# Kernel optimization log

Measured on AMD Instinct MI355X. Metric: run time of the kernel, lower is better.

## Reference

```python
import jax, jax.numpy as jnp
import numpy as np

B, CIN, L = 4, 128, 2048
D_MODEL, D_STATE, EXPAND, HEADDIM, NGROUPS = 256, 16, 3, 3, 1
D_INNER = EXPAND * D_MODEL            # 768
NHEADS = D_INNER // HEADDIM           # 256
CONV_DIM = D_INNER + 2 * NGROUPS * D_STATE   # 800
D_IN_PROJ = 2 * D_INNER + 2 * NGROUPS * D_STATE + NHEADS  # 1824
K_PROJ, D_CONV = 4, 4
EPS = 1e-5


def setup_inputs() -> dict:
    key = jax.random.key(0)
    ks = jax.random.split(key, 9)
    x = jax.random.normal(ks[0], (B, CIN, L), jnp.float32)
    proj_w = jax.random.normal(ks[1], (D_MODEL, CIN, K_PROJ), jnp.float32) / np.float32(np.sqrt(CIN * K_PROJ))
    in_proj_w = jax.random.normal(ks[2], (D_IN_PROJ, D_MODEL), jnp.float32) / np.float32(np.sqrt(D_MODEL))
    conv_w = jax.random.normal(ks[3], (CONV_DIM, 1, D_CONV), jnp.float32) / np.float32(np.sqrt(D_CONV))
    conv_b = jax.random.normal(ks[4], (CONV_DIM,), jnp.float32) * 0.01
    # dt_bias = inverse-softplus of dt ~ LogUniform[1e-3, 1e-1] (mamba2 init)
    u = jax.random.uniform(ks[5], (NHEADS,), jnp.float32)
    dt = jnp.exp(u * np.float32(np.log(0.1) - np.log(1e-3)) + np.float32(np.log(1e-3)))
    dt_bias = dt + jnp.log(-jnp.expm1(-dt))
    A_log = jnp.log(1.0 + 15.0 * jax.random.uniform(ks[6], (NHEADS,), jnp.float32))  # A in [-16,-1]
    D_skip = jnp.ones((NHEADS,), jnp.float32)
    norm_w = jnp.ones((D_INNER,), jnp.float32)
    out_proj_w = jax.random.normal(ks[7], (D_MODEL, D_INNER), jnp.float32) / np.float32(np.sqrt(D_INNER))
    return {"x": x, "proj_w": proj_w, "in_proj_w": in_proj_w, "conv_w": conv_w,
            "conv_b": conv_b, "dt_bias": dt_bias, "A_log": A_log, "D_skip": D_skip,
            "norm_w": norm_w, "out_proj_w": out_proj_w}


def _forward(x, proj_w, in_proj_w, conv_w, conv_b, dt_bias, A_log, D_skip, norm_w, out_proj_w):
    # outer Conv1d, padding='same' (k=4 -> left 1, right 2), no bias: (B,CIN,L)->(B,D_MODEL,L)
    h = jax.lax.conv_general_dilated(x, proj_w, (1,), [(1, 2)],
                                     dimension_numbers=("NCH", "OIH", "NCH"))
    u = h.transpose(0, 2, 1)                          # (B, L, d_model)
    zxbcdt = jnp.einsum("bld,ed->ble", u, in_proj_w)  # (B, L, 1824)
    z = zxbcdt[..., :D_INNER]                                     # (B,L,768)
    xBC = zxbcdt[..., D_INNER:D_INNER + CONV_DIM]                 # (B,L,800)
    dt = zxbcdt[..., D_INNER + CONV_DIM:]                         # (B,L,256)
    dt = jax.nn.softplus(dt + dt_bias)
    # depthwise causal conv (pad d_conv-1 on left) + SiLU
    xBC_c = jax.lax.conv_general_dilated(xBC.transpose(0, 2, 1), conv_w, (1,), [(D_CONV - 1, 0)],
                                         feature_group_count=CONV_DIM,
                                         dimension_numbers=("NCH", "OIH", "NCH"))
    xBC = jax.nn.silu(xBC_c + conv_b[None, :, None]).transpose(0, 2, 1)  # (B,L,800)
    xs = xBC[..., :D_INNER].reshape(B, L, NHEADS, HEADDIM)        # (B,L,H,P)
    Bm = xBC[..., D_INNER:D_INNER + D_STATE]                      # (B,L,N) (ngroups=1)
    Cm = xBC[..., D_INNER + D_STATE:]                             # (B,L,N)
    A = -jnp.exp(A_log)                                           # (H,)

    def step(hst, inp):
        dt_t, x_t, B_t, C_t = inp                 # (B,H),(B,H,P),(B,N),(B,N)
        dA = jnp.exp(dt_t * A)[:, :, None, None]  # (B,H,1,1)
        hst = dA * hst + jnp.einsum("bh,bhp,bn->bhpn", dt_t, x_t, B_t)
        y_t = jnp.einsum("bhpn,bn->bhp", hst, C_t)
        return hst, y_t

    h0 = jnp.zeros((B, NHEADS, HEADDIM, D_STATE), x.dtype)
    _, ys = jax.lax.scan(step, h0, (dt.transpose(1, 0, 2), xs.transpose(1, 0, 2, 3),
                                    Bm.transpose(1, 0, 2), Cm.transpose(1, 0, 2)))
    y = ys.transpose(1, 0, 2, 3) + D_skip[None, None, :, None] * xs   # (B,L,H,P)
    y = y.reshape(B, L, D_INNER)
    # gated RMSNorm: gate first, then normalize (norm_before_gate=False)
    y = y * jax.nn.silu(z)
    y = y * jax.lax.rsqrt(jnp.mean(y * y, axis=-1, keepdims=True) + EPS) * norm_w
    out = jnp.einsum("ble,de->bld", y, out_proj_w)   # (B,L,d_model)
    return out.transpose(0, 2, 1)                    # (B,d_model,L)


def reference(x, proj_w, in_proj_w, conv_w, conv_b, dt_bias, A_log, D_skip, norm_w, out_proj_w):
    return _forward(x, proj_w, in_proj_w, conv_w, conv_b, dt_bias, A_log, D_skip, norm_w, out_proj_w)
```

## Files before the change

kernel.cpp:

```cpp
#include <hip/hip_runtime.h>
#include <hip/hip_fp16.h>
#include <math.h>

#define B_     4
#define CIN    128
#define LEN    2048
#define DMODEL 256
#define DSTATE 16
#define NHEADS 256
#define DINNER 768
#define CONVDIM 800
#define DINPROJ 1824
#define EPS_   1e-5f
#define CHUNK  64
#define NCHUNK 32

typedef _Float16 f16x8 __attribute__((ext_vector_type(8)));
typedef float    f32x4 __attribute__((ext_vector_type(4)));

__device__ __forceinline__ float silu_(float x){ return x / (1.0f + __expf(-x)); }
__device__ __forceinline__ float softplus_(float x){
    return x > 0.f ? x + log1pf(__expf(-x)) : log1pf(__expf(x));
}

__device__ __forceinline__ void gl2lds16(const _Float16* g, _Float16* l){
    __builtin_amdgcn_global_load_lds(
        (const __attribute__((address_space(1))) void*)g,
        (__attribute__((address_space(3))) void*)l, 16, 0, 0);
}

__global__ __launch_bounds__(256) void k_f2h(const float* __restrict__ a,
                                             _Float16* __restrict__ o, int n){
    for (int i = blockIdx.x * 256 + threadIdx.x; i < n; i += gridDim.x * 256)
        o[i] = (_Float16)a[i];
}

__global__ __launch_bounds__(256) void k_im2col(const float* __restrict__ x,
                                                _Float16* __restrict__ xcol){
    __shared__ float xs[CIN][68];
    int blk = blockIdx.x;
    int b  = blk >> 5;
    int l0 = (blk & 31) << 6;
    const float* xb = x + (size_t)b * CIN * LEN;
    for (int idx = threadIdx.x; idx < CIN * 67; idx += 256){
        int ci = idx / 67, j = idx % 67;
        int gl = l0 - 1 + j;
        xs[ci][j] = (gl >= 0 && gl < LEN) ? xb[ci * LEN + gl] : 0.f;
    }
    __syncthreads();
    #pragma unroll
    for (int v = 0; v < 16; v++){
        int id = v * 256 + threadIdx.x;
        int rl = id >> 6, c = id & 63;
        f16x8 pk;
        #pragma unroll
        for (int e = 0; e < 8; e++){
            int ci = c * 2 + (e >> 2), k = e & 3;
            pk[e] = (_Float16)xs[ci][rl + k];
        }
        *(f16x8*)&xcol[((size_t)(b * LEN + l0 + rl)) * 512 + c * 8] = pk;
    }
}

template<int K, int EPI>
__global__ __launch_bounds__(256) void k_gemm(const _Float16* __restrict__ A,
                                              const _Float16* __restrict__ Bw,
                                              const float* __restrict__ dt_bias,
                                              _Float16* __restrict__ o_u,
                                              _Float16* __restrict__ o_z,
                                              _Float16* __restrict__ o_xbc,
                                              _Float16* __restrict__ o_dt,
                                              float* __restrict__ o_f){
    __shared__ __align__(16) _Float16 As[128 * 32];
    __shared__ __align__(16) _Float16 Bs[128 * 32];
    int tid  = threadIdx.x;
    int wv   = tid >> 6;
    int lane = tid & 63;
    int quad = lane >> 4;
    int l16  = lane & 15;
    int m0 = blockIdx.x * 128;
    int n0 = blockIdx.y * 128;
    int wm = (wv >> 1) * 64;
    int wn = (wv & 1) * 64;
    int srow = lane >> 2;
    int scol = (lane & 3) * 8;

    f32x4 acc[4][4];
    #pragma unroll
    for (int i = 0; i < 4; i++)
        #pragma unroll
        for (int j = 0; j < 4; j++)
            acc[i][j] = (f32x4){0.f, 0.f, 0.f, 0.f};

    for (int k0 = 0; k0 < K; k0 += 32){
        #pragma unroll
        for (int j = 0; j < 2; j++){
            int ar = m0 + wv * 32 + j * 16 + srow;
            gl2lds16(A + (size_t)ar * K + k0 + scol,
                     &As[(wv * 32 + j * 16) * 32]);
            int nr = n0 + wv * 32 + j * 16 + srow;
            if (EPI == 1) nr = nr > (DINPROJ - 1) ? (DINPROJ - 1) : nr;
            gl2lds16(Bw + (size_t)nr * K + k0 + scol,
                     &Bs[(wv * 32 + j * 16) * 32]);
        }
        __syncthreads();
        f16x8 af[4], bf[4];
        #pragma unroll
        for (int i = 0; i < 4; i++)
            af[i] = *(const f16x8*)&As[(wm + i * 16 + l16) * 32 + quad * 8];
        #pragma unroll
        for (int j = 0; j < 4; j++)
            bf[j] = *(const f16x8*)&Bs[(wn + j * 16 + l16) * 32 + quad * 8];
        #pragma unroll
        for (int i = 0; i < 4; i++)
            #pragma unroll
            for (int j = 0; j < 4; j++)
                acc[i][j] = __builtin_amdgcn_mfma_f32_16x16x32_f16(
                                af[i], bf[j], acc[i][j], 0, 0, 0);
        __syncthreads();
    }

    if (EPI == 0){
        #pragma unroll
        for (int j = 0; j < 4; j++){
            int col = n0 + wn + j * 16 + l16;
            #pragma unroll
            for (int i = 0; i < 4; i++){
                int row = m0 + wm + i * 16 + quad * 4;
                #pragma unroll
                for (int r = 0; r < 4; r++)
                    o_u[(size_t)(row + r) * DMODEL + col] = (_Float16)acc[i][j][r];
            }
        }
    } else if (EPI == 1){
        #pragma unroll
        for (int j = 0; j < 4; j++){
            int col = n0 + wn + j * 16 + l16;
            if (col < DINNER){
                #pragma unroll
                for (int i = 0; i < 4; i++){
                    int row = m0 + wm + i * 16 + quad * 4;
                    #pragma unroll
                    for (int r = 0; r < 4; r++)
                        o_z[(size_t)(row + r) * DINNER + col] = (_Float16)acc[i][j][r];
                }
            } else if (col < DINNER + CONVDIM){
                int cc = col - DINNER;
                #pragma unroll
                for (int i = 0; i < 4; i++){
                    int row = m0 + wm + i * 16 + quad * 4;
                    #pragma unroll
                    for (int r = 0; r < 4; r++)
                        o_xbc[(size_t)(row + r) * CONVDIM + cc] = (_Float16)acc[i][j][r];
                }
            } else if (col < DINPROJ){
                int hh = col - (DINNER + CONVDIM);
                float bias = dt_bias[hh];
                #pragma unroll
                for (int i = 0; i < 4; i++){
                    int row = m0 + wm + i * 16 + quad * 4;
                    #pragma unroll
                    for (int r = 0; r < 4; r++)
                        o_dt[(size_t)(row + r) * NHEADS + hh] =
                            (_Float16)softplus_(acc[i][j][r] + bias);
                }
            }
        }
    } else {
        #pragma unroll
        for (int i = 0; i < 4; i++){
            int row = m0 + wm + i * 16 + quad * 4;
            int b = row >> 11, l = row & (LEN - 1);
            #pragma unroll
            for (int j = 0; j < 4; j++){
                int d = n0 + wn + j * 16 + l16;
                *(f32x4*)&o_f[(((size_t)(b * DMODEL + d)) << 11) + l] = acc[i][j];
            }
        }
    }
}

__global__ __launch_bounds__(256) void k_dwconv(const __half* __restrict__ xbc,
                                                const float* __restrict__ cw,
                                                const float* __restrict__ cb,
                                                __half* __restrict__ xcc){
    int idx = blockIdx.x * 256 + threadIdx.x;
    int c = idx % CONVDIM;
    int r = idx / CONVDIM;
    int l = r & (LEN - 1);
    float4 wv = *(const float4*)(cw + c * 4);
    float acc = cb[c];
    if (l >= 3){
        const __half* base = xbc + (size_t)(r - 3) * CONVDIM + c;
        acc += __half2float(base[0]) * wv.x + __half2float(base[CONVDIM]) * wv.y +
               __half2float(base[2 * CONVDIM]) * wv.z + __half2float(base[3 * CONVDIM]) * wv.w;
    } else {
        const float wk[4] = {wv.x, wv.y, wv.z, wv.w};
        for (int k = 0; k < 4; k++){
            int t = l - 3 + k;
            if (t >= 0) acc += __half2float(xbc[(size_t)(r + k - 3) * CONVDIM + c]) * wk[k];
        }
    }
    xcc[idx] = __float2half(silu_(acc));
}

__global__ __launch_bounds__(64) void k_scanA(const __half* __restrict__ dtb,
                                              const __half* __restrict__ xcc,
                                              const float* __restrict__ A_log,
                                              __half* __restrict__ cstate,
                                              float* __restrict__ dsum){
    int blk = blockIdx.x;
    int c  = blk & (NCHUNK - 1);
    int hg = (blk >> 5) & 63;
    int b  = blk >> 11;
    int lane = threadIdx.x;
    int hl = lane >> 4;
    int n  = lane & 15;
    int h  = hg * 4 + hl;
    int c0 = h * 3;
    float A = -__expf(A_log[h]);
    int t0 = c * CHUNK;
    const __half* xr  = xcc + ((size_t)b * LEN + t0) * CONVDIM;
    const __half* dtp = dtb + ((size_t)b * LEN + t0) * NHEADS + h;
    float h0 = 0.f, h1 = 0.f, h2 = 0.f, sdt = 0.f;
    for (int t = 0; t < CHUNK; t++){
        float vx0 = __half2float(xr[c0]);
        float vx1 = __half2float(xr[c0 + 1]);
        float vx2 = __half2float(xr[c0 + 2]);
        float vB  = __half2float(xr[DINNER + n]);
        float cdt = __half2float(dtp[(size_t)t * NHEADS]);
        float dA  = __expf(cdt * A);
        float dtB = cdt * vB;
        h0 = fmaf(h0, dA, vx0 * dtB);
        h1 = fmaf(h1, dA, vx1 * dtB);
        h2 = fmaf(h2, dA, vx2 * dtB);
        sdt += cdt;
        xr += CONVDIM;
    }
    size_t sbase = (((size_t)(b * NHEADS + h)) * NCHUNK + c) * 48;
    cstate[sbase + n]      = __float2half(h0);
    cstate[sbase + 16 + n] = __float2half(h1);
    cstate[sbase + 32 + n] = __float2half(h2);
    if (n == 0) dsum[(size_t)(b * NHEADS + h) * NCHUNK + c] = __expf(A * sdt);
}

__global__ __launch_bounds__(64) void k_scanB(__half* __restrict__ cstate,
                                              const float* __restrict__ dsum){
    int bh = blockIdx.x;
    int lane = threadIdx.x;
    if (lane >= 48) return;
    __half* st = cstate + (size_t)bh * NCHUNK * 48 + lane;
    const float* dd = dsum + (size_t)bh * NCHUNK;
    float H = 0.f;
    for (int c = 0; c < NCHUNK; c++){
        float d = dd[c];
        float s = __half2float(st[(size_t)c * 48]);
        st[(size_t)c * 48] = __float2half(H);
        H = fmaf(H, d, s);
    }
}

__global__ __launch_bounds__(64) void k_scanC(const __half* __restrict__ dtb,
                                              const __half* __restrict__ xcc,
                                              const float* __restrict__ A_log,
                                              const float* __restrict__ D_skip,
                                              const __half* __restrict__ cstate,
                                              __half* __restrict__ y){
    int blk = blockIdx.x;
    int c  = blk & (NCHUNK - 1);
    int hg = (blk >> 5) & 63;
    int b  = blk >> 11;
    int lane = threadIdx.x;
    int hl = lane >> 4;
    int n  = lane & 15;
    int h  = hg * 4 + hl;
    int c0 = h * 3;
    float A   = -__expf(A_log[h]);
    float Dsk = D_skip[h];
    int t0 = c * CHUNK;
    const __half* xr  = xcc + ((size_t)b * LEN + t0) * CONVDIM;
    const __half* dtp = dtb + ((size_t)b * LEN + t0) * NHEADS + h;
    size_t sbase = (((size_t)(b * NHEADS + h)) * NCHUNK + c) * 48;
    float h0 = __half2float(cstate[sbase + n]);
    float h1 = __half2float(cstate[sbase + 16 + n]);
    float h2 = __half2float(cstate[sbase + 32 + n]);
    __half* yp = y + ((size_t)b * LEN + t0) * DINNER + c0;
    for (int t = 0; t < CHUNK; t++){
        float vx0 = __half2float(xr[c0]);
        float vx1 = __half2float(xr[c0 + 1]);
        float vx2 = __half2float(xr[c0 + 2]);
        float vB  = __half2float(xr[DINNER + n]);
        float vC  = __half2float(xr[DINNER + DSTATE + n]);
        float cdt = __half2float(dtp[(size_t)t * NHEADS]);
        float dA  = __expf(cdt * A);
        float dtB = cdt * vB;
        h0 = fmaf(h0, dA, vx0 * dtB);
        h1 = fmaf(h1, dA, vx1 * dtB);
        h2 = fmaf(h2, dA, vx2 * dtB);
        float p0 = h0 * vC, p1 = h1 * vC, p2 = h2 * vC;
        #pragma unroll
        for (int m = 1; m < 16; m <<= 1){
            p0 += __shfl_xor(p0, m, 64);
            p1 += __shfl_xor(p1, m, 64);
            p2 += __shfl_xor(p2, m, 64);
        }
        if (n < 3){
            float pv = (n == 0) ? p0 : ((n == 1) ? p1 : p2);
            float xv = (n == 0) ? vx0 : ((n == 1) ? vx1 : vx2);
            yp[n] = __float2half(fmaf(Dsk, xv, pv));
        }
        xr += CONVDIM;
        yp += DINNER;
    }
}

__global__ __launch_bounds__(256) void k_norm(__half* __restrict__ y,
                                              const __half* __restrict__ z,
                                              const float* __restrict__ nw){
    __shared__ float wsum[4];
    size_t r = blockIdx.x;
    int tid = threadIdx.x;
    const __half* zr = z + r * DINNER;
    __half* yr = y + r * DINNER;
    int e0 = tid, e1 = tid + 256, e2 = tid + 512;
    float t0 = __half2float(yr[e0]) * silu_(__half2float(zr[e0]));
    float t1 = __half2float(yr[e1]) * silu_(__half2float(zr[e1]));
    float t2 = __half2float(yr[e2]) * silu_(__half2float(zr[e2]));
    float ss = t0 * t0 + t1 * t1 + t2 * t2;
    #pragma unroll
    for (int m = 1; m < 64; m <<= 1) ss += __shfl_xor(ss, m, 64);
    if ((tid & 63) == 0) wsum[tid >> 6] = ss;
    __syncthreads();
    float tot = wsum[0] + wsum[1] + wsum[2] + wsum[3];
    float sc = rsqrtf(tot / (float)DINNER + EPS_);
    yr[e0] = __float2half(t0 * sc * nw[e0]);
    yr[e1] = __float2half(t1 * sc * nw[e1]);
    yr[e2] = __float2half(t2 * sc * nw[e2]);
}

extern "C" void kernel_launch(void* const* d_in, const int* in_sizes, int n_in,
                              void* d_out, int out_size, void* d_ws, size_t ws_size,
                              hipStream_t stream) {
    const float* x          = (const float*)d_in[0];
    const float* proj_w     = (const float*)d_in[1];
    const float* in_proj_w  = (const float*)d_in[2];
    const float* conv_w     = (const float*)d_in[3];
    const float* conv_b     = (const float*)d_in[4];
    const float* dt_bias    = (const float*)d_in[5];
    const float* A_log      = (const float*)d_in[6];
    const float* D_skip     = (const float*)d_in[7];
    const float* norm_w     = (const float*)d_in[8];
    const float* out_proj_w = (const float*)d_in[9];
    float* out = (float*)d_out;

    char* ob = (char*)d_out;
    _Float16* pw_h  = (_Float16*)ob;
    _Float16* ipw_h = (_Float16*)(ob + 262144);

    char* wsb = (char*)d_ws;
    _Float16* xcol  = (_Float16*)(wsb);
    _Float16* u_h   = (_Float16*)(wsb + 8388608);
    __half*   xcc_h = (__half*)(wsb);
    __half*   z_h   = (__half*)(wsb + 13107200);
    __half*   xbc_h = (__half*)(wsb + 25690112);
    __half*   y_h   = xbc_h;
    __half*   dt_h  = (__half*)(wsb + 38797312);
    __half*   cstate= (__half*)(wsb + 42991616);
    float*    dsum  = (float*)(wsb + 46137344);
    _Float16* opw_h = (_Float16*)(wsb + 46268416);

    k_f2h   <<<64, 256, 0, stream>>>(proj_w,     pw_h,  DMODEL * CIN * 4);
    k_f2h   <<<64, 256, 0, stream>>>(in_proj_w,  ipw_h, DINPROJ * DMODEL);
    k_f2h   <<<64, 256, 0, stream>>>(out_proj_w, opw_h, DMODEL * DINNER);
    k_im2col<<<128, 256, 0, stream>>>(x, xcol);
    k_gemm<512, 0><<<dim3(64, 2), 256, 0, stream>>>(xcol, pw_h, nullptr,
        u_h, nullptr, nullptr, nullptr, nullptr);
    k_gemm<256, 1><<<dim3(64, 15), 256, 0, stream>>>(u_h, ipw_h, dt_bias,
        nullptr, (_Float16*)z_h, (_Float16*)xbc_h, (_Float16*)dt_h, nullptr);
    k_dwconv<<<25600, 256, 0, stream>>>(xbc_h, conv_w, conv_b, xcc_h);
    k_scanA <<<8192, 64, 0, stream>>>(dt_h, xcc_h, A_log, cstate, dsum);
    k_scanB <<<1024, 64, 0, stream>>>(cstate, dsum);
    k_scanC <<<8192, 64, 0, stream>>>(dt_h, xcc_h, A_log, D_skip, cstate, y_h);
    k_norm  <<<8192, 256, 0, stream>>>(y_h, z_h, norm_w);
    k_gemm<768, 2><<<dim3(64, 2), 256, 0, stream>>>((const _Float16*)y_h, opw_h,
        nullptr, nullptr, nullptr, nullptr, nullptr, out);
}
```

Before: 318.4 us.

## Fuse intra-chunk output into chunk-state scan and add parallel inter-chunk correction

The first scan pass now also produces the intra-chunk output y (from a zero initial state), staging B/C, x and dt for the chunk in shared memory rather than doing strided global loads every step. The second sequential scan pass over all chunks is replaced by a parallel correction kernel: one thread per timestep takes a prefix sum of dt, computes the decay from the chunk's carried-in state, and adds C·H·decay to y. This removes one full sequential recurrence pass, at the cost of an extra read-modify-write of y in fp16 and a shuffle reduction added to the first pass.

```diff
diff --git a/kernel.cpp b/kernel.cpp
--- a/kernel.cpp
+++ b/kernel.cpp
@@ -204,11 +204,16 @@
     xcc[idx] = __float2half(silu_(acc));
 }
 
-__global__ __launch_bounds__(64) void k_scanA(const __half* __restrict__ dtb,
-                                              const __half* __restrict__ xcc,
-                                              const float* __restrict__ A_log,
-                                              __half* __restrict__ cstate,
-                                              float* __restrict__ dsum){
+__global__ __launch_bounds__(64) void k_scanAY(const __half* __restrict__ dtb,
+                                               const __half* __restrict__ xcc,
+                                               const float* __restrict__ A_log,
+                                               const float* __restrict__ D_skip,
+                                               __half* __restrict__ y,
+                                               __half* __restrict__ cstate,
+                                               float* __restrict__ dsum){
+    __shared__ __align__(16) __half sBC[CHUNK * 32];
+    __shared__ __align__(8)  __half sx[CHUNK * 12];
+    __shared__ __align__(8)  __half sdt4[CHUNK * 4];
     int blk = blockIdx.x;
     int c  = blk & (NCHUNK - 1);
     int hg = (blk >> 5) & 63;
@@ -217,25 +222,60 @@
     int hl = lane >> 4;
     int n  = lane & 15;
     int h  = hg * 4 + hl;
-    int c0 = h * 3;
-    float A = -__expf(A_log[h]);
     int t0 = c * CHUNK;
-    const __half* xr  = xcc + ((size_t)b * LEN + t0) * CONVDIM;
-    const __half* dtp = dtb + ((size_t)b * LEN + t0) * NHEADS + h;
+    size_t row0 = (size_t)(b * LEN + t0);
+
+    {
+        const char* g = (const char*)xcc + (row0 * CONVDIM + DINNER) * 2;
+        int tt = lane >> 2, q = lane & 3;
+        #pragma unroll
+        for (int i = 0; i < 4; i++)
+            gl2lds16((const _Float16*)(g + (size_t)(i * 16 + tt) * (CONVDIM * 2) + q * 16),
+                     (_Float16*)&sBC[i * 512]);
+    }
+    {
+        const char* gx = (const char*)xcc + (row0 + lane) * (CONVDIM * 2) + hg * 24;
+        uint2 a0 = *(const uint2*)(gx);
+        uint2 a1 = *(const uint2*)(gx + 8);
+        uint2 a2 = *(const uint2*)(gx + 16);
+        *(uint2*)&sx[lane * 12]     = a0;
+        *(uint2*)&sx[lane * 12 + 4] = a1;
+        *(uint2*)&sx[lane * 12 + 8] = a2;
+        const char* gd = (const char*)dtb + (row0 + lane) * (NHEADS * 2) + hg * 8;
+        *(uint2*)&sdt4[lane * 4] = *(const uint2*)gd;
+    }
+    __syncthreads();
+
+    float A   = -__expf(A_log[h]);
+    float Dsk = D_skip[h];
     float h0 = 0.f, h1 = 0.f, h2 = 0.f, sdt = 0.f;
+    __half* yp = y + row0 * DINNER + hg * 12 + hl * 3;
+    #pragma unroll 4
     for (int t = 0; t < CHUNK; t++){
-        float vx0 = __half2float(xr[c0]);
-        float vx1 = __half2float(xr[c0 + 1]);
-        float vx2 = __half2float(xr[c0 + 2]);
-        float vB  = __half2float(xr[DINNER + n]);
-        float cdt = __half2float(dtp[(size_t)t * NHEADS]);
+        float vx0 = __half2float(sx[t * 12 + hl * 3]);
+        float vx1 = __half2float(sx[t * 12 + hl * 3 + 1]);
+        float vx2 = __half2float(sx[t * 12 + hl * 3 + 2]);
+        float vB  = __half2float(sBC[t * 32 + n]);
+        float vC  = __half2float(sBC[t * 32 + 16 + n]);
+        float cdt = __half2float(sdt4[t * 4 + hl]);
         float dA  = __expf(cdt * A);
         float dtB = cdt * vB;
         h0 = fmaf(h0, dA, vx0 * dtB);
         h1 = fmaf(h1, dA, vx1 * dtB);
         h2 = fmaf(h2, dA, vx2 * dtB);
         sdt += cdt;
-        xr += CONVDIM;
+        float p0 = h0 * vC, p1 = h1 * vC, p2 = h2 * vC;
+        p0 += __shfl_xor(p0, 1, 64); p1 += __shfl_xor(p1, 1, 64); p2 += __shfl_xor(p2, 1, 64);
+        p0 += __shfl_xor(p0, 2, 64); p1 += __shfl_xor(p1, 2, 64); p2 += __shfl_xor(p2, 2, 64);
+        int g = n & 3;
+        float q = (g == 1) ? p1 : ((g == 2) ? p2 : p0);
+        q += __shfl_xor(q, 4, 64);
+        q += __shfl_xor(q, 8, 64);
+        if (n < 3){
+            float xv = (n == 0) ? vx0 : ((n == 1) ? vx1 : vx2);
+            yp[n] = __float2half(fmaf(Dsk, xv, q));
+        }
+        yp += DINNER;
     }
     size_t sbase = (((size_t)(b * NHEADS + h)) * NCHUNK + c) * 48;
     cstate[sbase + n]      = __float2half(h0);
@@ -260,58 +300,43 @@
     }
 }
 
-__global__ __launch_bounds__(64) void k_scanC(const __half* __restrict__ dtb,
-                                              const __half* __restrict__ xcc,
-                                              const float* __restrict__ A_log,
-                                              const float* __restrict__ D_skip,
-                                              const __half* __restrict__ cstate,
-                                              __half* __restrict__ y){
-    int blk = blockIdx.x;
-    int c  = blk & (NCHUNK - 1);
-    int hg = (blk >> 5) & 63;
-    int b  = blk >> 11;
+__global__ __launch_bounds__(64) void k_corr(const __half* __restrict__ dtb,
+                                             const __half* __restrict__ xcc,
+                                             const float* __restrict__ A_log,
+                                             const __half* __restrict__ cstate,
+                                             __half* __restrict__ y){
+    __shared__ float sH[48];
+    int c = 1 + blockIdx.x;
+    int h = blockIdx.y;
+    int b = blockIdx.z;
     int lane = threadIdx.x;
-    int hl = lane >> 4;
-    int n  = lane & 15;
-    int h  = hg * 4 + hl;
-    int c0 = h * 3;
-    float A   = -__expf(A_log[h]);
-    float Dsk = D_skip[h];
+    size_t sbase = (((size_t)(b * NHEADS + h)) * NCHUNK + c) * 48;
+    if (lane < 48) sH[lane] = __half2float(cstate[sbase + lane]);
+    float A = -__expf(A_log[h]);
     int t0 = c * CHUNK;
-    const __half* xr  = xcc + ((size_t)b * LEN + t0) * CONVDIM;
-    const __half* dtp = dtb + ((size_t)b * LEN + t0) * NHEADS + h;
-    size_t sbase = (((size_t)(b * NHEADS + h)) * NCHUNK + c) * 48;
-    float h0 = __half2float(cstate[sbase + n]);
-    float h1 = __half2float(cstate[sbase + 16 + n]);
-    float h2 = __half2float(cstate[sbase + 32 + n]);
-    __half* yp = y + ((size_t)b * LEN + t0) * DINNER + c0;
-    for (int t = 0; t < CHUNK; t++){
-        float vx0 = __half2float(xr[c0]);
-        float vx1 = __half2float(xr[c0 + 1]);
-        float vx2 = __half2float(xr[c0 + 2]);
-        float vB  = __half2float(xr[DINNER + n]);
-        float vC  = __half2float(xr[DINNER + DSTATE + n]);
-        float cdt = __half2float(dtp[(size_t)t * NHEADS]);
-        float dA  = __expf(cdt * A);
-        float dtB = cdt * vB;
-        h0 = fmaf(h0, dA, vx0 * dtB);
-        h1 = fmaf(h1, dA, vx1 * dtB);
-        h2 = fmaf(h2, dA, vx2 * dtB);
-        float p0 = h0 * vC, p1 = h1 * vC, p2 = h2 * vC;
-        #pragma unroll
-        for (int m = 1; m < 16; m <<= 1){
-            p0 += __shfl_xor(p0, m, 64);
-            p1 += __shfl_xor(p1, m, 64);
-            p2 += __shfl_xor(p2, m, 64);
-        }
-        if (n < 3){
-            float pv = (n == 0) ? p0 : ((n == 1) ? p1 : p2);
-            float xv = (n == 0) ? vx0 : ((n == 1) ? vx1 : vx2);
-            yp[n] = __float2half(fmaf(Dsk, xv, pv));
-        }
-        xr += CONVDIM;
-        yp += DINNER;
-    }
+    size_t row = (size_t)(b * LEN + t0 + lane);
+    float cdt = __half2float(dtb[row * NHEADS + h]);
+    float cum = cdt;
+    #pragma unroll
+    for (int m = 1; m < 64; m <<= 1){
+        float v = __shfl_up(cum, m, 64);
+        if (lane >= m) cum += v;
+    }
+    float decay = __expf(A * cum);
+    __syncthreads();
+    const __half* Cp = xcc + row * CONVDIM + DINNER + DSTATE;
+    float c0 = 0.f, c1 = 0.f, c2 = 0.f;
+    #pragma unroll
+    for (int nn = 0; nn < 16; nn++){
+        float cv = __half2float(Cp[nn]);
+        c0 = fmaf(cv, sH[nn],      c0);
+        c1 = fmaf(cv, sH[16 + nn], c1);
+        c2 = fmaf(cv, sH[32 + nn], c2);
+    }
+    __half* yy = y + row * DINNER + h * 3;
+    yy[0] = __float2half(fmaf(decay, c0, __half2float(yy[0])));
+    yy[1] = __float2half(fmaf(decay, c1, __half2float(yy[1])));
+    yy[2] = __float2half(fmaf(decay, c2, __half2float(yy[2])));
 }
 
 __global__ __launch_bounds__(256) void k_norm(__half* __restrict__ y,
@@ -378,9 +403,9 @@
     k_gemm<256, 1><<<dim3(64, 15), 256, 0, stream>>>(u_h, ipw_h, dt_bias,
         nullptr, (_Float16*)z_h, (_Float16*)xbc_h, (_Float16*)dt_h, nullptr);
     k_dwconv<<<25600, 256, 0, stream>>>(xbc_h, conv_w, conv_b, xcc_h);
-    k_scanA <<<8192, 64, 0, stream>>>(dt_h, xcc_h, A_log, cstate, dsum);
+    k_scanAY<<<8192, 64, 0, stream>>>(dt_h, xcc_h, A_log, D_skip, y_h, cstate, dsum);
     k_scanB <<<1024, 64, 0, stream>>>(cstate, dsum);
-    k_scanC <<<8192, 64, 0, stream>>>(dt_h, xcc_h, A_log, D_skip, cstate, y_h);
+    k_corr  <<<dim3(NCHUNK - 1, NHEADS, B_), 64, 0, stream>>>(dt_h, xcc_h, A_log, cstate, y_h);
     k_norm  <<<8192, 256, 0, stream>>>(y_h, z_h, norm_w);
     k_gemm<768, 2><<<dim3(64, 2), 256, 0, stream>>>((const _Float16*)y_h, opw_h,
         nullptr, nullptr, nullptr, nullptr, nullptr, out);
```

After: 408.0 us. 1.28x slower.

## Replace sequential chunk scan with SSD-style intra-band quadratic form and correction pass

Applied to the files above, without the earlier changes.

Replaces the per-timestep sequential scan kernels with a chunked SSD formulation. Each block loads a 64-row band and 64 heads into LDS. It computes cumulative decay, C·B dot products, and the intra-band output with 16-step sub-segments plus sub-segment state carries. It also writes band end states and per-row decay factors (E0, stored in the output buffer as scratch) so a separate correction kernel can add the inter-band contribution. The D-skip term moves into the norm kernel. This trades the latency-bound serial recurrence over tiny 64-thread blocks for parallel, arithmetic-heavy work, at the cost of more exp evaluations, high register pressure, and extra E0 traffic.

```diff
diff --git a/kernel.cpp b/kernel.cpp
--- a/kernel.cpp
+++ b/kernel.cpp
@@ -12,10 +12,12 @@
 #define CONVDIM 800
 #define DINPROJ 1824
 #define EPS_   1e-5f
-#define CHUNK  64
-#define NCHUNK 32
+#define BAND   64
+#define NBAND  32
+#define SEG    16
 
 typedef _Float16 f16x8 __attribute__((ext_vector_type(8)));
+typedef _Float16 f16x4 __attribute__((ext_vector_type(4)));
 typedef float    f32x4 __attribute__((ext_vector_type(4)));
 
 __device__ __forceinline__ float silu_(float x){ return x / (1.0f + __expf(-x)); }
@@ -204,44 +206,236 @@
     xcc[idx] = __float2half(silu_(acc));
 }
 
-__global__ __launch_bounds__(64) void k_scanA(const __half* __restrict__ dtb,
-                                              const __half* __restrict__ xcc,
-                                              const float* __restrict__ A_log,
-                                              __half* __restrict__ cstate,
-                                              float* __restrict__ dsum){
-    int blk = blockIdx.x;
-    int c  = blk & (NCHUNK - 1);
-    int hg = (blk >> 5) & 63;
-    int b  = blk >> 11;
-    int lane = threadIdx.x;
-    int hl = lane >> 4;
-    int n  = lane & 15;
-    int h  = hg * 4 + hl;
-    int c0 = h * 3;
-    float A = -__expf(A_log[h]);
-    int t0 = c * CHUNK;
-    const __half* xr  = xcc + ((size_t)b * LEN + t0) * CONVDIM;
-    const __half* dtp = dtb + ((size_t)b * LEN + t0) * NHEADS + h;
-    float h0 = 0.f, h1 = 0.f, h2 = 0.f, sdt = 0.f;
-    for (int t = 0; t < CHUNK; t++){
-        float vx0 = __half2float(xr[c0]);
-        float vx1 = __half2float(xr[c0 + 1]);
-        float vx2 = __half2float(xr[c0 + 2]);
-        float vB  = __half2float(xr[DINNER + n]);
-        float cdt = __half2float(dtp[(size_t)t * NHEADS]);
-        float dA  = __expf(cdt * A);
-        float dtB = cdt * vB;
-        h0 = fmaf(h0, dA, vx0 * dtB);
-        h1 = fmaf(h1, dA, vx1 * dtB);
-        h2 = fmaf(h2, dA, vx2 * dtB);
-        sdt += cdt;
-        xr += CONVDIM;
-    }
-    size_t sbase = (((size_t)(b * NHEADS + h)) * NCHUNK + c) * 48;
-    cstate[sbase + n]      = __float2half(h0);
-    cstate[sbase + 16 + n] = __float2half(h1);
-    cstate[sbase + 32 + n] = __float2half(h2);
-    if (n == 0) dsum[(size_t)(b * NHEADS + h) * NCHUNK + c] = __expf(A * sdt);
+__global__ __launch_bounds__(256) void k_y(const __half* __restrict__ dtb,
+                                           const __half* __restrict__ xcc,
+                                           const float* __restrict__ A_log,
+                                           __half* __restrict__ y,
+                                           float* __restrict__ E0,
+                                           __half* __restrict__ cstate,
+                                           float* __restrict__ dsum){
+    __shared__ __align__(16) char smem[59392];
+    __half* sBC = (__half*)smem;
+    __half* sX  = (__half*)(smem + 4096);
+    __half* sHL = (__half*)(smem + 4096);
+    __half* sDT = (__half*)(smem + 28672);
+    float*  sA  = (float*)(smem + 36864);
+    float*  sG  = (float*)(smem + 54272);
+
+    int band = blockIdx.x, hq = blockIdx.y, b = blockIdx.z;
+    int row0 = band * BAND;
+    int tid = threadIdx.x;
+    int wv = tid >> 6, lane = tid & 63;
+
+    {
+        int c = wv, slot = c * 64 + lane;
+        int row = slot >> 2, off = slot & 3;
+        gl2lds16((const _Float16*)((const char*)xcc +
+                   (size_t)(b * LEN + row0 + row) * 1600 + 1536 + off * 16),
+                 (_Float16*)(smem + c * 1024));
+    }
+    #pragma unroll
+    for (int i = 0; i < 6; i++){
+        int c = wv + i * 4, slot = c * 64 + lane;
+        int row = slot / 24, off = slot % 24;
+        gl2lds16((const _Float16*)((const char*)xcc +
+                   (size_t)(b * LEN + row0 + row) * 1600 + hq * 384 + off * 16),
+                 (_Float16*)(smem + 4096 + c * 1024));
+    }
+    #pragma unroll
+    for (int i = 0; i < 2; i++){
+        int c = wv + i * 4, slot = c * 64 + lane;
+        int row = slot >> 3, off = slot & 7;
+        gl2lds16((const _Float16*)((const char*)dtb +
+                   (size_t)(b * LEN + row0 + row) * 512 + hq * 128 + off * 16),
+                 (_Float16*)(smem + 28672 + c * 1024));
+    }
+    __syncthreads();
+
+    if (tid < 64){
+        int h = tid;
+        float A = -__expf(A_log[hq * 64 + h]);
+        float cum = 0.f;
+        for (int tt = 0; tt < 64; tt++){
+            cum += (float)sDT[tt * 64 + h];
+            sA[tt * 68 + h] = A * cum;
+        }
+    } else if (tid < 128){
+        int base = tid - 64;
+        #pragma unroll
+        for (int i = 0; i < 16; i++){
+            int e = base + i * 64;
+            int tt = e >> 4, ss = e & 15;
+            int s = (tt & 48) + ss;
+            f16x8 ca = *(const f16x8*)&sBC[tt * 32 + 16];
+            f16x8 cb = *(const f16x8*)&sBC[tt * 32 + 24];
+            f16x8 ba = *(const f16x8*)&sBC[s * 32];
+            f16x8 bb = *(const f16x8*)&sBC[s * 32 + 8];
+            float acc = 0.f;
+            #pragma unroll
+            for (int n = 0; n < 8; n++)
+                acc += (float)ca[n] * (float)ba[n] + (float)cb[n] * (float)bb[n];
+            sG[tt * 20 + ss] = acc;
+        }
+    } else {
+        int base = tid - 128;
+        #pragma unroll
+        for (int i = 0; i < 32; i++){
+            int p = base + i * 128;
+            int tt = p >> 6, h = p & 63;
+            float dtv = (float)sDT[tt * 64 + h];
+            int xi = tt * 192 + h * 3;
+            sX[xi]     = __float2half((float)sX[xi]     * dtv);
+            sX[xi + 1] = __float2half((float)sX[xi + 1] * dtv);
+            sX[xi + 2] = __float2half((float)sX[xi + 2] * dtv);
+        }
+    }
+    __syncthreads();
+
+    int t = tid >> 2, hsub = tid & 3, Hb = hsub * 16;
+    int tmod = t & 15, tseg = t & 48;
+
+    f32x4 atv[4];
+    #pragma unroll
+    for (int k4 = 0; k4 < 4; k4++)
+        atv[k4] = *(const f32x4*)&sA[t * 68 + Hb + k4 * 4];
+
+    {
+        float* E0p = E0 + ((size_t)(b * LEN + row0 + t)) * 256 + hq * 64 + Hb;
+        #pragma unroll
+        for (int k4 = 0; k4 < 4; k4++){
+            f32x4 ev;
+            #pragma unroll
+            for (int j = 0; j < 4; j++) ev[j] = __expf(atv[k4][j]);
+            *(f32x4*)&E0p[k4 * 4] = ev;
+        }
+    }
+
+    float y0[16], y1[16], y2[16];
+    #pragma unroll
+    for (int i = 0; i < 16; i++){ y0[i] = 0.f; y1[i] = 0.f; y2[i] = 0.f; }
+
+    for (int ss = 0; ss < 16; ss++){
+        int s = tseg + ss;
+        float g = sG[t * 20 + ss];
+        bool valid = (ss <= tmod);
+        f32x4 av[4];
+        #pragma unroll
+        for (int k4 = 0; k4 < 4; k4++)
+            av[k4] = *(const f32x4*)&sA[s * 68 + Hb + k4 * 4];
+        f16x8 xv[6];
+        #pragma unroll
+        for (int c = 0; c < 6; c++)
+            xv[c] = *(const f16x8*)&sX[s * 192 + Hb * 3 + c * 8];
+        #pragma unroll
+        for (int k4 = 0; k4 < 4; k4++)
+            #pragma unroll
+            for (int j = 0; j < 4; j++){
+                int hh = k4 * 4 + j;
+                float d = fminf(atv[k4][j] - av[k4][j], 0.f);
+                float w = __expf(d) * g;
+                w = valid ? w : 0.f;
+                y0[hh] = fmaf(w, (float)xv[(hh*3+0)>>3][(hh*3+0)&7], y0[hh]);
+                y1[hh] = fmaf(w, (float)xv[(hh*3+1)>>3][(hh*3+1)&7], y1[hh]);
+                y2[hh] = fmaf(w, (float)xv[(hh*3+2)>>3][(hh*3+2)&7], y2[hh]);
+            }
+    }
+
+    int h2 = tid >> 2, ng = tid & 3;
+    float F[4][12];
+    float aeK[4];
+    #pragma unroll
+    for (int k = 0; k < 4; k++){
+        float ae = sA[(k * 16 + 15) * 68 + h2];
+        aeK[k] = ae;
+        #pragma unroll
+        for (int i = 0; i < 12; i++) F[k][i] = 0.f;
+        for (int ss = 0; ss < 16; ss++){
+            int s = k * 16 + ss;
+            float e = __expf(ae - sA[s * 68 + h2]);
+            f16x4 bv = *(const f16x4*)&sBC[s * 32 + ng * 4];
+            float x0 = (float)sX[s * 192 + h2 * 3];
+            float x1 = (float)sX[s * 192 + h2 * 3 + 1];
+            float x2 = (float)sX[s * 192 + h2 * 3 + 2];
+            #pragma unroll
+            for (int nn = 0; nn < 4; nn++){
+                float wb = e * (float)bv[nn];
+                F[k][nn*3+0] = fmaf(wb, x0, F[k][nn*3+0]);
+                F[k][nn*3+1] = fmaf(wb, x1, F[k][nn*3+1]);
+                F[k][nn*3+2] = fmaf(wb, x2, F[k][nn*3+2]);
+            }
+        }
+    }
+
+    __syncthreads();
+
+    {
+        float hc[12];
+        #pragma unroll
+        for (int i = 0; i < 12; i++) hc[i] = F[0][i];
+        #pragma unroll
+        for (int i = 0; i < 12; i++)
+            sHL[(0 * 64 + h2) * 48 + ng * 12 + i] = __float2half(hc[i]);
+        #pragma unroll
+        for (int k = 1; k <= 2; k++){
+            float D = __expf(aeK[k] - aeK[k-1]);
+            #pragma unroll
+            for (int i = 0; i < 12; i++) hc[i] = fmaf(D, hc[i], F[k][i]);
+            #pragma unroll
+            for (int i = 0; i < 12; i++)
+                sHL[(k * 64 + h2) * 48 + ng * 12 + i] = __float2half(hc[i]);
+        }
+        float D3 = __expf(aeK[3] - aeK[2]);
+        __half* cp = cstate + ((size_t)((b * 256 + hq * 64 + h2) * NBAND + band)) * 48 + ng * 12;
+        #pragma unroll
+        for (int i = 0; i < 12; i++)
+            cp[i] = __float2half(fmaf(D3, hc[i], F[3][i]));
+        if (ng == 0)
+            dsum[(size_t)(b * 256 + hq * 64 + h2) * NBAND + band] = __expf(aeK[3]);
+    }
+    __syncthreads();
+
+    {
+        f16x8 cva = *(const f16x8*)&sBC[t * 32 + 16];
+        f16x8 cvb = *(const f16x8*)&sBC[t * 32 + 24];
+        int k = t >> 4;
+        if (k > 0){
+            const float* arow = &sA[(k * 16 - 1) * 68];
+            #pragma unroll
+            for (int k4 = 0; k4 < 4; k4++)
+                #pragma unroll
+                for (int j = 0; j < 4; j++){
+                    int hh = k4 * 4 + j, h = Hb + hh;
+                    float e = __expf(atv[k4][j] - arow[h]);
+                    const __half* hl = &sHL[((k - 1) * 64 + h) * 48];
+                    f16x8 hv[6];
+                    #pragma unroll
+                    for (int c = 0; c < 6; c++) hv[c] = *(const f16x8*)&hl[c * 8];
+                    float a0 = 0.f, a1 = 0.f, a2 = 0.f;
+                    #pragma unroll
+                    for (int n = 0; n < 16; n++){
+                        float cn = (n < 8) ? (float)cva[n & 7] : (float)cvb[n & 7];
+                        a0 = fmaf(cn, (float)hv[(n*3+0)>>3][(n*3+0)&7], a0);
+                        a1 = fmaf(cn, (float)hv[(n*3+1)>>3][(n*3+1)&7], a1);
+                        a2 = fmaf(cn, (float)hv[(n*3+2)>>3][(n*3+2)&7], a2);
+                    }
+                    y0[hh] = fmaf(e, a0, y0[hh]);
+                    y1[hh] = fmaf(e, a1, y1[hh]);
+                    y2[hh] = fmaf(e, a2, y2[hh]);
+                }
+        }
+        __half* yp = y + (size_t)(b * LEN + row0 + t) * DINNER + hq * 192 + hsub * 48;
+        #pragma unroll
+        for (int c = 0; c < 6; c++){
+            f16x8 pk;
+            #pragma unroll
+            for (int e2 = 0; e2 < 8; e2++){
+                int gi = c * 8 + e2;
+                int hh = gi / 3, p = gi % 3;
+                pk[e2] = (_Float16)(p == 0 ? y0[hh] : (p == 1 ? y1[hh] : y2[hh]));
+            }
+            *(f16x8*)&yp[c * 8] = pk;
+        }
+    }
 }
 
 __global__ __launch_bounds__(64) void k_scanB(__half* __restrict__ cstate,
@@ -249,10 +443,10 @@
     int bh = blockIdx.x;
     int lane = threadIdx.x;
     if (lane >= 48) return;
-    __half* st = cstate + (size_t)bh * NCHUNK * 48 + lane;
-    const float* dd = dsum + (size_t)bh * NCHUNK;
+    __half* st = cstate + (size_t)bh * NBAND * 48 + lane;
+    const float* dd = dsum + (size_t)bh * NBAND;
     float H = 0.f;
-    for (int c = 0; c < NCHUNK; c++){
+    for (int c = 0; c < NBAND; c++){
         float d = dd[c];
         float s = __half2float(st[(size_t)c * 48]);
         st[(size_t)c * 48] = __float2half(H);
@@ -260,72 +454,109 @@
     }
 }
 
-__global__ __launch_bounds__(64) void k_scanC(const __half* __restrict__ dtb,
+__global__ __launch_bounds__(256) void k_corr(const float* __restrict__ E0,
                                               const __half* __restrict__ xcc,
-                                              const float* __restrict__ A_log,
-                                              const float* __restrict__ D_skip,
                                               const __half* __restrict__ cstate,
                                               __half* __restrict__ y){
-    int blk = blockIdx.x;
-    int c  = blk & (NCHUNK - 1);
-    int hg = (blk >> 5) & 63;
-    int b  = blk >> 11;
-    int lane = threadIdx.x;
-    int hl = lane >> 4;
-    int n  = lane & 15;
-    int h  = hg * 4 + hl;
-    int c0 = h * 3;
-    float A   = -__expf(A_log[h]);
-    float Dsk = D_skip[h];
-    int t0 = c * CHUNK;
-    const __half* xr  = xcc + ((size_t)b * LEN + t0) * CONVDIM;
-    const __half* dtp = dtb + ((size_t)b * LEN + t0) * NHEADS + h;
-    size_t sbase = (((size_t)(b * NHEADS + h)) * NCHUNK + c) * 48;
-    float h0 = __half2float(cstate[sbase + n]);
-    float h1 = __half2float(cstate[sbase + 16 + n]);
-    float h2 = __half2float(cstate[sbase + 32 + n]);
-    __half* yp = y + ((size_t)b * LEN + t0) * DINNER + c0;
-    for (int t = 0; t < CHUNK; t++){
-        float vx0 = __half2float(xr[c0]);
-        float vx1 = __half2float(xr[c0 + 1]);
-        float vx2 = __half2float(xr[c0 + 2]);
-        float vB  = __half2float(xr[DINNER + n]);
-        float vC  = __half2float(xr[DINNER + DSTATE + n]);
-        float cdt = __half2float(dtp[(size_t)t * NHEADS]);
-        float dA  = __expf(cdt * A);
-        float dtB = cdt * vB;
-        h0 = fmaf(h0, dA, vx0 * dtB);
-        h1 = fmaf(h1, dA, vx1 * dtB);
-        h2 = fmaf(h2, dA, vx2 * dtB);
-        float p0 = h0 * vC, p1 = h1 * vC, p2 = h2 * vC;
-        #pragma unroll
-        for (int m = 1; m < 16; m <<= 1){
-            p0 += __shfl_xor(p0, m, 64);
-            p1 += __shfl_xor(p1, m, 64);
-            p2 += __shfl_xor(p2, m, 64);
-        }
-        if (n < 3){
-            float pv = (n == 0) ? p0 : ((n == 1) ? p1 : p2);
-            float xv = (n == 0) ? vx0 : ((n == 1) ? vx1 : vx2);
-            yp[n] = __float2half(fmaf(Dsk, xv, pv));
-        }
-        xr += CONVDIM;
-        yp += DINNER;
+    __shared__ __align__(16) char smem[24576];
+    __half* sC  = (__half*)smem;
+    __half* sHI = (__half*)(smem + 2048);
+    float*  sE0 = (float*)(smem + 8192);
+
+    int band = blockIdx.x, hq = blockIdx.y, b = blockIdx.z;
+    int row0 = band * BAND;
+    int tid = threadIdx.x;
+    int wv = tid >> 6, lane = tid & 63;
+
+    #pragma unroll
+    for (int i = 0; i < 6; i++){
+        int m = wv * 6 + i;
+        if (m < 2){
+            int slot = m * 64 + lane, row = slot >> 1, off = slot & 1;
+            gl2lds16((const _Float16*)((const char*)xcc +
+                       (size_t)(b * LEN + row0 + row) * 1600 + 1568 + off * 16),
+                     (_Float16*)(smem + m * 1024));
+        } else if (m < 8){
+            int mm = m - 2, slot = mm * 64 + lane;
+            int h = slot / 6, off = slot % 6;
+            gl2lds16((const _Float16*)((const char*)cstate +
+                       ((size_t)((b * 256 + hq * 64 + h) * NBAND + band)) * 96 + off * 16),
+                     (_Float16*)(smem + 2048 + mm * 1024));
+        } else {
+            int mm = m - 8, slot = mm * 64 + lane;
+            int row = slot >> 4, off = slot & 15;
+            gl2lds16((const _Float16*)((const char*)E0 +
+                       (size_t)(b * LEN + row0 + row) * 1024 + hq * 256 + off * 16),
+                     (_Float16*)(smem + 8192 + mm * 1024));
+        }
+    }
+    __syncthreads();
+
+    int t = tid >> 2, hsub = tid & 3, Hb = hsub * 16;
+    f16x8 cva = *(const f16x8*)&sC[t * 16];
+    f16x8 cvb = *(const f16x8*)&sC[t * 16 + 8];
+    f32x4 e0v[4];
+    #pragma unroll
+    for (int k4 = 0; k4 < 4; k4++)
+        e0v[k4] = *(const f32x4*)&sE0[t * 64 + Hb + k4 * 4];
+
+    __half* yp = y + (size_t)(b * LEN + row0 + t) * DINNER + hq * 192 + hsub * 48;
+    f16x8 yv[6];
+    #pragma unroll
+    for (int c = 0; c < 6; c++) yv[c] = *(const f16x8*)&yp[c * 8];
+    float o[48];
+    #pragma unroll
+    for (int c = 0; c < 6; c++)
+        #pragma unroll
+        for (int e2 = 0; e2 < 8; e2++) o[c * 8 + e2] = (float)yv[c][e2];
+
+    #pragma unroll
+    for (int k4 = 0; k4 < 4; k4++)
+        #pragma unroll
+        for (int j = 0; j < 4; j++){
+            int hh = k4 * 4 + j, h = Hb + hh;
+            const __half* hl = &sHI[h * 48];
+            f16x8 hv[6];
+            #pragma unroll
+            for (int c = 0; c < 6; c++) hv[c] = *(const f16x8*)&hl[c * 8];
+            float a0 = 0.f, a1 = 0.f, a2 = 0.f;
+            #pragma unroll
+            for (int n = 0; n < 16; n++){
+                float cn = (n < 8) ? (float)cva[n & 7] : (float)cvb[n & 7];
+                a0 = fmaf(cn, (float)hv[(n*3+0)>>3][(n*3+0)&7], a0);
+                a1 = fmaf(cn, (float)hv[(n*3+1)>>3][(n*3+1)&7], a1);
+                a2 = fmaf(cn, (float)hv[(n*3+2)>>3][(n*3+2)&7], a2);
+            }
+            float e0 = e0v[k4][j];
+            o[hh*3+0] = fmaf(e0, a0, o[hh*3+0]);
+            o[hh*3+1] = fmaf(e0, a1, o[hh*3+1]);
+            o[hh*3+2] = fmaf(e0, a2, o[hh*3+2]);
+        }
+
+    #pragma unroll
+    for (int c = 0; c < 6; c++){
+        f16x8 pk;
+        #pragma unroll
+        for (int e2 = 0; e2 < 8; e2++) pk[e2] = (_Float16)o[c * 8 + e2];
+        *(f16x8*)&yp[c * 8] = pk;
     }
 }
 
 __global__ __launch_bounds__(256) void k_norm(__half* __restrict__ y,
                                               const __half* __restrict__ z,
+                                              const __half* __restrict__ xcc,
+                                              const float* __restrict__ D_skip,
                                               const float* __restrict__ nw){
     __shared__ float wsum[4];
     size_t r = blockIdx.x;
     int tid = threadIdx.x;
     const __half* zr = z + r * DINNER;
+    const __half* xr = xcc + r * CONVDIM;
     __half* yr = y + r * DINNER;
     int e0 = tid, e1 = tid + 256, e2 = tid + 512;
-    float t0 = __half2float(yr[e0]) * silu_(__half2float(zr[e0]));
-    float t1 = __half2float(yr[e1]) * silu_(__half2float(zr[e1]));
-    float t2 = __half2float(yr[e2]) * silu_(__half2float(zr[e2]));
+    float t0 = (__half2float(yr[e0]) + D_skip[e0/3]*__half2float(xr[e0])) * silu_(__half2float(zr[e0]));
+    float t1 = (__half2float(yr[e1]) + D_skip[e1/3]*__half2float(xr[e1])) * silu_(__half2float(zr[e1]));
+    float t2 = (__half2float(yr[e2]) + D_skip[e2/3]*__half2float(xr[e2])) * silu_(__half2float(zr[e2]));
     float ss = t0 * t0 + t1 * t1 + t2 * t2;
     #pragma unroll
     for (int m = 1; m < 64; m <<= 1) ss += __shfl_xor(ss, m, 64);
@@ -356,6 +587,7 @@
     char* ob = (char*)d_out;
     _Float16* pw_h  = (_Float16*)ob;
     _Float16* ipw_h = (_Float16*)(ob + 262144);
+    float*    E0    = (float*)d_out;
 
     char* wsb = (char*)d_ws;
     _Float16* xcol  = (_Float16*)(wsb);
@@ -378,10 +610,11 @@
     k_gemm<256, 1><<<dim3(64, 15), 256, 0, stream>>>(u_h, ipw_h, dt_bias,
         nullptr, (_Float16*)z_h, (_Float16*)xbc_h, (_Float16*)dt_h, nullptr);
     k_dwconv<<<25600, 256, 0, stream>>>(xbc_h, conv_w, conv_b, xcc_h);
-    k_scanA <<<8192, 64, 0, stream>>>(dt_h, xcc_h, A_log, cstate, dsum);
+    k_y     <<<dim3(NBAND, 4, B_), 256, 0, stream>>>(dt_h, xcc_h, A_log,
+                                                     y_h, E0, cstate, dsum);
     k_scanB <<<1024, 64, 0, stream>>>(cstate, dsum);
-    k_scanC <<<8192, 64, 0, stream>>>(dt_h, xcc_h, A_log, D_skip, cstate, y_h);
-    k_norm  <<<8192, 256, 0, stream>>>(y_h, z_h, norm_w);
+    k_corr  <<<dim3(NBAND, 4, B_), 256, 0, stream>>>(E0, xcc_h, cstate, y_h);
+    k_norm  <<<8192, 256, 0, stream>>>(y_h, z_h, xcc_h, D_skip, norm_w);
     k_gemm<768, 2><<<dim3(64, 2), 256, 0, stream>>>((const _Float16*)y_h, opw_h,
         nullptr, nullptr, nullptr, nullptr, nullptr, out);
 }
```

Measured after the change: 295.0 us. -7.3%, faster.
